# Kernel optimization log

Hardware: AMD Instinct MI355X
Metric: run time of the kernel (lower is better)

The kernel has to match this reference:

```python
import jax, jax.numpy as jnp
import numpy as np

N = 50000   # nodes
E = 800000  # edges
B = 64      # graphs in batch
IN = 128    # in_features
HID = 64    # hidden_channels
H = 4       # head_count
C = 10      # out_classes
NEG = 0.2   # leaky relu negative slope
EPS = 1e-5  # batchnorm eps (eval mode, running mean 0 / var 1)


def _gat(x, edge_index, W, a_src, a_dst, b):
    """PyG GATConv (add_self_loops=False, concat=True), eval mode (no dropout)."""
    Hh, F = a_src.shape
    xW = (x @ W).reshape(-1, Hh, F)                       # [N,H,F]
    src, dst = edge_index[0], edge_index[1]
    e = (jnp.einsum('nhf,hf->nh', xW, a_src)[src]
         + jnp.einsum('nhf,hf->nh', xW, a_dst)[dst])      # [E,H]
    e = jnp.where(e > 0, e, NEG * e)                      # leaky relu
    m = jax.ops.segment_max(e, dst, num_segments=N)       # per-dst max
    m = jnp.where(jnp.isfinite(m), m, 0.0)
    p = jnp.exp(e - m[dst])
    denom = jax.ops.segment_sum(p, dst, num_segments=N)
    alpha = p / jnp.maximum(denom[dst], 1e-16)            # edge softmax over dst
    out = jax.ops.segment_sum(alpha[:, :, None] * xW[src], dst, num_segments=N)
    return out.reshape(-1, Hh * F) + b


def _bn_relu(y, g, be):
    # BatchNorm1d in eval mode with running_mean=0, running_var=1, then ReLU
    return jax.nn.relu(g * y / jnp.sqrt(1.0 + EPS) + be)


def setup_inputs():
    key = jax.random.key(0)
    ks = jax.random.split(key, 24)
    s = lambda k, shape: (jax.random.normal(k, shape, jnp.float32) * 0.05)
    z = lambda shape: jnp.zeros(shape, jnp.float32)
    o = lambda shape: jnp.ones(shape, jnp.float32)
    return {
        'acc_flag': 0,
        'x': jax.random.normal(ks[0], (N, IN), jnp.float32),
        'edge_index': jax.random.randint(ks[1], (2, E), 0, N),
        'batch': jnp.sort(jax.random.randint(ks[2], (N,), 0, B)),
        # layer 1: GATConv(IN -> HID, heads=H, concat)
        'W1': s(ks[3], (IN, H * HID)), 'a_src1': s(ks[4], (H, HID)), 'a_dst1': s(ks[5], (H, HID)), 'b1': z((H * HID,)),
        # proj: GATConv(H*HID -> HID, heads=1) + BN
        'W2': s(ks[6], (H * HID, HID)), 'a_src2': s(ks[7], (1, HID)), 'a_dst2': s(ks[8], (1, HID)), 'b2': z((HID,)), 'g2': o((HID,)), 'be2': z((HID,)),
        # block 1
        'W3': s(ks[9], (HID, HID)), 'a_src3': s(ks[10], (1, HID)), 'a_dst3': s(ks[11], (1, HID)), 'b3': z((HID,)), 'g3': o((HID,)), 'be3': z((HID,)),
        # block 2
        'W4': s(ks[12], (HID, HID)), 'a_src4': s(ks[13], (1, HID)), 'a_dst4': s(ks[14], (1, HID)), 'b4': z((HID,)), 'g4': o((HID,)), 'be4': z((HID,)),
        # MLP head
        'Wh1': s(ks[15], (HID, 128)), 'bh1': z((128,)),
        'Wh2': s(ks[16], (128, C)), 'bh2': z((C,)),
    }


def reference(acc_flag, x, edge_index, batch,
              W1, a_src1, a_dst1, b1,
              W2, a_src2, a_dst2, b2, g2, be2,
              W3, a_src3, a_dst3, b3, g3, be3,
              W4, a_src4, a_dst4, b4, g4, be4,
              Wh1, bh1, Wh2, bh2):
    # hardware GAT layer + ReLU (relu applied twice in original -> idempotent)
    x1 = jax.nn.relu(_gat(x, edge_index, W1, a_src1, a_dst1, b1))   # [N, H*HID]
    # projection block: residual base is zeros (shape mismatch H*HID vs HID)
    h = _bn_relu(_gat(x1, edge_index, W2, a_src2, a_dst2, b2), g2, be2)
    # residual blocks (shapes match -> x + relu(bn(y)))
    h = h + _bn_relu(_gat(h, edge_index, W3, a_src3, a_dst3, b3), g3, be3)
    h = h + _bn_relu(_gat(h, edge_index, W4, a_src4, a_dst4, b4), g4, be4)
    # global mean pool over graphs
    pooled = jax.ops.segment_sum(h, batch, num_segments=B)
    cnt = jnp.maximum(jax.ops.segment_sum(jnp.ones((N,), h.dtype), batch, num_segments=B), 1.0)
    hp = pooled / cnt[:, None]                                      # [B, HID]
    # MLP head
    return jax.nn.relu(hp @ Wh1 + bh1) @ Wh2 + bh2                  # [B, C]
```

## Files before the change

### kernel.cpp

```cpp
#include <hip/hip_runtime.h>

#define N_NODES 50000
#define N_EDGES 800000
#define N_GRAPHS 64
#define F_IN 128
#define F_HID 64
#define N_HEADS 4
#define N_CLASSES 10
#define NEG_SLOPE 0.2f
#define BN_RSQ 0.9999950000374997f

typedef __bf16 bf16x8 __attribute__((ext_vector_type(8)));
typedef float floatx4 __attribute__((ext_vector_type(4)));

__device__ __forceinline__ float lrelu(float v) { return v > 0.0f ? v : NEG_SLOPE * v; }

__device__ __forceinline__ float b2f(unsigned short u) {
    return __uint_as_float(((unsigned int)u) << 16);
}
__device__ __forceinline__ unsigned short f2b(float f) {
    unsigned int u = __float_as_uint(f);
    return (unsigned short)((u + 0x7fffu + ((u >> 16) & 1u)) >> 16);
}
__device__ __forceinline__ float blo(unsigned int d) { return __uint_as_float(d << 16); }
__device__ __forceinline__ float bhi(unsigned int d) { return __uint_as_float(d & 0xffff0000u); }

__global__ void k_deg(const int* __restrict__ ei, int* __restrict__ deg) {
    int e = blockIdx.x * blockDim.x + threadIdx.x;
    if (e < N_EDGES) atomicAdd(&deg[ei[N_EDGES + e]], 1);
}

__global__ void k_offs(const int* __restrict__ deg, int* __restrict__ offs,
                       int* __restrict__ total) {
    int i = blockIdx.x * blockDim.x + threadIdx.x;
    int lane = threadIdx.x & 63;
    int v = (i < N_NODES) ? deg[i] : 0;
    int incl = v;
    for (int o = 1; o < 64; o <<= 1) {
        int t = __shfl_up(incl, o);
        if (lane >= o) incl += t;
    }
    int wtot = __shfl(incl, 63);
    int base = 0;
    if (lane == 0) base = atomicAdd(total, wtot);
    base = __shfl(base, 0);
    if (i < N_NODES) offs[i] = base + incl - v;
}

__global__ void k_fill(const int* __restrict__ ei, const int* __restrict__ offs,
                       int* __restrict__ cur, int* __restrict__ csr_src) {
    int e = blockIdx.x * blockDim.x + threadIdx.x;
    if (e < N_EDGES) {
        int d = ei[N_EDGES + e];
        int pos = offs[d] + atomicAdd(&cur[d], 1);
        csr_src[pos] = ei[e];
    }
}

__global__ void k_bounds(const int* __restrict__ batch, int* __restrict__ bounds) {
    int g = threadIdx.x;
    if (g > N_GRAPHS) return;
    int lo = 0, hi = N_NODES;
    while (lo < hi) {
        int mid = (lo + hi) >> 1;
        if (batch[mid] < g) lo = mid + 1; else hi = mid;
    }
    bounds[g] = lo;
}

__global__ void k_prepw(const float* __restrict__ W, unsigned short* __restrict__ Wt,
                        int K, int N) {
    int i = blockIdx.x * blockDim.x + threadIdx.x;
    if (i < K * N) {
        int k = i / N, n = i % N;
        Wt[n * K + k] = f2b(W[i]);
    }
}

template <int K, int N, bool AF32>
__global__ __launch_bounds__(256) void k_mgemm(const void* __restrict__ Ap,
                                               const unsigned short* __restrict__ Bt,
                                               unsigned short* __restrict__ out,
                                               int rows) {
    constexpr int LDP = K + 8;
    __shared__ unsigned short As[64 * LDP];
    const int tid = threadIdx.x;
    const int r0 = blockIdx.x * 64;
    if (AF32) {
        const float* A = (const float*)Ap;
        for (int i = tid; i < 16 * K; i += 256) {
            int r = i / (K / 4), c4 = i % (K / 4);
            int row = r0 + r;
            float4 v = (row < rows) ? *(const float4*)&A[(size_t)row * K + c4 * 4]
                                    : make_float4(0.f, 0.f, 0.f, 0.f);
            ushort4 u;
            u.x = f2b(v.x); u.y = f2b(v.y); u.z = f2b(v.z); u.w = f2b(v.w);
            *(ushort4*)&As[r * LDP + c4 * 4] = u;
        }
    } else {
        const unsigned short* A = (const unsigned short*)Ap;
        for (int i = tid; i < 8 * K; i += 256) {
            int r = i / (K / 8), c8 = i % (K / 8);
            int row = r0 + r;
            uint4 v;
            if (row < rows) v = *(const uint4*)&A[(size_t)row * K + c8 * 8];
            else { v.x = v.y = v.z = v.w = 0; }
            *(uint4*)&As[r * LDP + c8 * 8] = v;
        }
    }
    __syncthreads();
    const int w = tid >> 6, lane = tid & 63;
    const int quad = lane >> 4, l16 = lane & 15;
    bf16x8 afrag[K / 32];
#pragma unroll
    for (int kk = 0; kk < K / 32; ++kk)
        afrag[kk] = *(const bf16x8*)&As[(w * 16 + l16) * LDP + kk * 32 + quad * 8];
#pragma unroll 1
    for (int ct = 0; ct < N / 16; ++ct) {
        floatx4 acc = {0.f, 0.f, 0.f, 0.f};
#pragma unroll
        for (int kk = 0; kk < K / 32; ++kk) {
            const bf16x8 bfrag =
                *(const bf16x8*)&Bt[(size_t)(ct * 16 + l16) * K + kk * 32 + quad * 8];
            acc = __builtin_amdgcn_mfma_f32_16x16x32_bf16(afrag[kk], bfrag, acc, 0, 0, 0);
        }
        const int gr0 = r0 + w * 16 + quad * 4;
        const int gc = ct * 16 + l16;
#pragma unroll
        for (int rg = 0; rg < 4; ++rg) {
            int gr = gr0 + rg;
            if (gr < rows) out[(size_t)gr * N + gc] = f2b(acc[rg]);
        }
    }
}

__global__ void k_dots4(const unsigned short* __restrict__ xW, const float* __restrict__ asrc,
                        const float* __restrict__ adst, float* __restrict__ es,
                        float* __restrict__ ed) {
    int w = (blockIdx.x * blockDim.x + threadIdx.x) >> 6;
    int lane = threadIdx.x & 63;
    if (w >= N_NODES) return;
    const ushort4 xu = *(const ushort4*)&xW[w * 256 + lane * 4];
    const float4 as = *(const float4*)&asrc[lane * 4];
    const float4 ad = *(const float4*)&adst[lane * 4];
    const float x0 = b2f(xu.x), x1 = b2f(xu.y), x2 = b2f(xu.z), x3 = b2f(xu.w);
    float ss = x0 * as.x + x1 * as.y + x2 * as.z + x3 * as.w;
    float dd = x0 * ad.x + x1 * ad.y + x2 * ad.z + x3 * ad.w;
    for (int off = 1; off < 16; off <<= 1) {
        ss += __shfl_xor(ss, off);
        dd += __shfl_xor(dd, off);
    }
    if ((lane & 15) == 0) {
        es[w * 4 + (lane >> 4)] = ss;
        ed[w * 4 + (lane >> 4)] = dd;
    }
}

__global__ void k_dots1(const unsigned short* __restrict__ xW, const float* __restrict__ asrc,
                        const float* __restrict__ adst, float* __restrict__ es,
                        float* __restrict__ ed) {
    int w = (blockIdx.x * blockDim.x + threadIdx.x) >> 6;
    int lane = threadIdx.x & 63;
    if (w >= N_NODES) return;
    float xv = b2f(xW[w * 64 + lane]);
    float ss = xv * asrc[lane];
    float dd = xv * adst[lane];
    for (int off = 1; off < 64; off <<= 1) {
        ss += __shfl_xor(ss, off);
        dd += __shfl_xor(dd, off);
    }
    if (lane == 0) { es[w] = ss; ed[w] = dd; }
}

__global__ __launch_bounds__(256) void k_gat1(
    const unsigned short* __restrict__ xW, const float* __restrict__ es, const float* __restrict__ ed,
    const int* __restrict__ offs, const int* __restrict__ deg, const int* __restrict__ csr,
    const float* __restrict__ bias, unsigned short* __restrict__ out) {
    __shared__ float ps[4][256];
    __shared__ int sbuf[4][64];
    const int wv = threadIdx.x >> 6;
    const int lane = threadIdx.x & 63;
    const int n = blockIdx.x * 4 + wv;
    if (n >= N_NODES) return;
    const int off = offs[n];
    const int dg = deg[n];
    const float4 edv = *(const float4*)&ed[n * 4];
    const int t = lane & 15, grp = lane >> 4, hq = t >> 2;

    float m0 = -3.0e38f, m1 = -3.0e38f, m2 = -3.0e38f, m3 = -3.0e38f;
    for (int i = lane; i < dg; i += 64) {
        int s = csr[off + i];
        const float4 ev = *(const float4*)&es[s * 4];
        m0 = fmaxf(m0, lrelu(ev.x + edv.x));
        m1 = fmaxf(m1, lrelu(ev.y + edv.y));
        m2 = fmaxf(m2, lrelu(ev.z + edv.z));
        m3 = fmaxf(m3, lrelu(ev.w + edv.w));
    }
    for (int o = 1; o < 64; o <<= 1) {
        m0 = fmaxf(m0, __shfl_xor(m0, o));
        m1 = fmaxf(m1, __shfl_xor(m1, o));
        m2 = fmaxf(m2, __shfl_xor(m2, o));
        m3 = fmaxf(m3, __shfl_xor(m3, o));
    }

    float acc[16];
#pragma unroll
    for (int k = 0; k < 16; ++k) acc[k] = 0.f;
    float d0 = 0.f, d1 = 0.f, d2 = 0.f, d3 = 0.f;

    for (int base = 0; base < dg; base += 64) {
        const int idx = base + lane;
        int s_l = 0;
        float p0 = 0.f, p1 = 0.f, p2 = 0.f, p3 = 0.f;
        if (idx < dg) {
            s_l = csr[off + idx];
            const float4 ev = *(const float4*)&es[s_l * 4];
            p0 = __expf(lrelu(ev.x + edv.x) - m0);
            p1 = __expf(lrelu(ev.y + edv.y) - m1);
            p2 = __expf(lrelu(ev.z + edv.z) - m2);
            p3 = __expf(lrelu(ev.w + edv.w) - m3);
        }
        d0 += p0; d1 += p1; d2 += p2; d3 += p3;
        *(float4*)&ps[wv][lane * 4] = make_float4(p0, p1, p2, p3);
        sbuf[wv][lane] = s_l;
        const int cnt = min(64, dg - base);
        for (int j4 = 0; j4 < cnt; j4 += 4) {
            const int j = j4 + grp;
            const float pj = ps[wv][j * 4 + hq];
            const int sj = sbuf[wv][j];
            const uint4 a = *(const uint4*)&xW[(size_t)sj * 256 + t * 16];
            const uint4 b = *(const uint4*)&xW[(size_t)sj * 256 + t * 16 + 8];
            acc[0]  = fmaf(pj, blo(a.x), acc[0]);
            acc[1]  = fmaf(pj, bhi(a.x), acc[1]);
            acc[2]  = fmaf(pj, blo(a.y), acc[2]);
            acc[3]  = fmaf(pj, bhi(a.y), acc[3]);
            acc[4]  = fmaf(pj, blo(a.z), acc[4]);
            acc[5]  = fmaf(pj, bhi(a.z), acc[5]);
            acc[6]  = fmaf(pj, blo(a.w), acc[6]);
            acc[7]  = fmaf(pj, bhi(a.w), acc[7]);
            acc[8]  = fmaf(pj, blo(b.x), acc[8]);
            acc[9]  = fmaf(pj, bhi(b.x), acc[9]);
            acc[10] = fmaf(pj, blo(b.y), acc[10]);
            acc[11] = fmaf(pj, bhi(b.y), acc[11]);
            acc[12] = fmaf(pj, blo(b.z), acc[12]);
            acc[13] = fmaf(pj, bhi(b.z), acc[13]);
            acc[14] = fmaf(pj, blo(b.w), acc[14]);
            acc[15] = fmaf(pj, bhi(b.w), acc[15]);
        }
    }
#pragma unroll
    for (int k = 0; k < 16; ++k) {
        acc[k] += __shfl_xor(acc[k], 16);
        acc[k] += __shfl_xor(acc[k], 32);
    }
    for (int o = 1; o < 64; o <<= 1) {
        d0 += __shfl_xor(d0, o);
        d1 += __shfl_xor(d1, o);
        d2 += __shfl_xor(d2, o);
        d3 += __shfl_xor(d3, o);
    }
    if (grp == 0) {
        const float dsel = hq == 0 ? d0 : hq == 1 ? d1 : hq == 2 ? d2 : d3;
        const float inv = 1.0f / fmaxf(dsel, 1e-16f);
#pragma unroll
        for (int k4 = 0; k4 < 16; k4 += 4) {
            const int c = t * 16 + k4;
            const float4 bv = *(const float4*)&bias[c];
            ushort4 o4;
            o4.x = f2b(fmaxf(fmaf(acc[k4 + 0], inv, bv.x), 0.f));
            o4.y = f2b(fmaxf(fmaf(acc[k4 + 1], inv, bv.y), 0.f));
            o4.z = f2b(fmaxf(fmaf(acc[k4 + 2], inv, bv.z), 0.f));
            o4.w = f2b(fmaxf(fmaf(acc[k4 + 3], inv, bv.w), 0.f));
            *(ushort4*)&out[(size_t)n * 256 + c] = o4;
        }
    }
}

template <bool RES>
__global__ __launch_bounds__(256) void k_gatL(
    const unsigned short* __restrict__ xW, const float* __restrict__ es, const float* __restrict__ ed,
    const int* __restrict__ offs, const int* __restrict__ deg, const int* __restrict__ csr,
    const float* __restrict__ bias, const float* __restrict__ gam, const float* __restrict__ bet,
    float* __restrict__ h, unsigned short* __restrict__ hb) {
    __shared__ float ps[4][64];
    __shared__ int sbuf[4][64];
    const int wv = threadIdx.x >> 6;
    const int lane = threadIdx.x & 63;
    const int n = blockIdx.x * 4 + wv;
    if (n >= N_NODES) return;
    const int off = offs[n];
    const int dg = deg[n];
    const float edn = ed[n];
    const int t = lane & 7, grp = lane >> 3;

    float m = -3.0e38f;
    for (int i = lane; i < dg; i += 64) {
        int s = csr[off + i];
        m = fmaxf(m, lrelu(es[s] + edn));
    }
    for (int o = 1; o < 64; o <<= 1) m = fmaxf(m, __shfl_xor(m, o));

    float acc[8];
#pragma unroll
    for (int k = 0; k < 8; ++k) acc[k] = 0.f;
    float dsum = 0.f;

    for (int base = 0; base < dg; base += 64) {
        const int idx = base + lane;
        int s_l = 0;
        float p_l = 0.f;
        if (idx < dg) {
            s_l = csr[off + idx];
            p_l = __expf(lrelu(es[s_l] + edn) - m);
        }
        dsum += p_l;
        ps[wv][lane] = p_l;
        sbuf[wv][lane] = s_l;
        const int cnt = min(64, dg - base);
        for (int j8 = 0; j8 < cnt; j8 += 8) {
            const int j = j8 + grp;
            const float pj = ps[wv][j];
            const int sj = sbuf[wv][j];
            const uint4 a = *(const uint4*)&xW[(size_t)sj * 64 + t * 8];
            acc[0] = fmaf(pj, blo(a.x), acc[0]);
            acc[1] = fmaf(pj, bhi(a.x), acc[1]);
            acc[2] = fmaf(pj, blo(a.y), acc[2]);
            acc[3] = fmaf(pj, bhi(a.y), acc[3]);
            acc[4] = fmaf(pj, blo(a.z), acc[4]);
            acc[5] = fmaf(pj, bhi(a.z), acc[5]);
            acc[6] = fmaf(pj, blo(a.w), acc[6]);
            acc[7] = fmaf(pj, bhi(a.w), acc[7]);
        }
    }
#pragma unroll
    for (int k = 0; k < 8; ++k) {
        acc[k] += __shfl_xor(acc[k], 8);
        acc[k] += __shfl_xor(acc[k], 16);
        acc[k] += __shfl_xor(acc[k], 32);
    }
    for (int o = 1; o < 64; o <<= 1) dsum += __shfl_xor(dsum, o);

    if (grp == 0) {
        const float inv = 1.0f / fmaxf(dsum, 1e-16f);
        const int c0 = t * 8;
        float hn[8];
#pragma unroll
        for (int k = 0; k < 8; ++k) {
            const int c = c0 + k;
            const float y = fmaf(acc[k], inv, bias[c]);
            const float z = fmaxf(fmaf(gam[c] * y, BN_RSQ, bet[c]), 0.f);
            hn[k] = RES ? h[(size_t)n * 64 + c] + z : z;
        }
        *(float4*)&h[(size_t)n * 64 + c0] = make_float4(hn[0], hn[1], hn[2], hn[3]);
        *(float4*)&h[(size_t)n * 64 + c0 + 4] = make_float4(hn[4], hn[5], hn[6], hn[7]);
        ushort4 u0, u1;
        u0.x = f2b(hn[0]); u0.y = f2b(hn[1]); u0.z = f2b(hn[2]); u0.w = f2b(hn[3]);
        u1.x = f2b(hn[4]); u1.y = f2b(hn[5]); u1.z = f2b(hn[6]); u1.w = f2b(hn[7]);
        *(ushort4*)&hb[(size_t)n * 64 + c0] = u0;
        *(ushort4*)&hb[(size_t)n * 64 + c0 + 4] = u1;
    }
}

__global__ __launch_bounds__(256) void k_pool2(const float* __restrict__ h,
                                               const int* __restrict__ bounds,
                                               float* __restrict__ hp) {
    __shared__ float part[4][64];
    const int g = blockIdx.x;
    const int lane = threadIdx.x & 63;
    const int wid = threadIdx.x >> 6;
    const int s = bounds[g], e = bounds[g + 1];
    float acc = 0.f;
    for (int n = s + wid; n < e; n += 4) acc += h[n * 64 + lane];
    part[wid][lane] = acc;
    __syncthreads();
    if (wid == 0) {
        float v = part[0][lane] + part[1][lane] + part[2][lane] + part[3][lane];
        hp[g * 64 + lane] = v / fmaxf((float)(e - s), 1.0f);
    }
}

__global__ __launch_bounds__(256) void k_head(const float* __restrict__ hpg,
                                              const float* __restrict__ Wh1,
                                              const float* __restrict__ bh1,
                                              const float* __restrict__ Wh2,
                                              const float* __restrict__ bh2,
                                              float* __restrict__ out) {
    __shared__ float hp[64 * 64];
    __shared__ float t1[64 * 128];
    const int tid = threadIdx.x;
    for (int i = tid; i < 64 * 64; i += 256) hp[i] = hpg[i];
    __syncthreads();
    for (int i = tid; i < 64 * 128; i += 256) {
        int g = i >> 7, j = i & 127;
        float s = bh1[j];
        for (int k = 0; k < 64; ++k) s = fmaf(hp[g * 64 + k], Wh1[k * 128 + j], s);
        t1[i] = fmaxf(s, 0.f);
    }
    __syncthreads();
    for (int i = tid; i < 640; i += 256) {
        int g = i / 10, j = i - g * 10;
        float s = bh2[j];
        for (int k = 0; k < 128; ++k) s = fmaf(t1[g * 128 + k], Wh2[k * 10 + j], s);
        out[i] = s;
    }
}

extern "C" void kernel_launch(void* const* d_in, const int* in_sizes, int n_in,
                              void* d_out, int out_size, void* d_ws, size_t ws_size,
                              hipStream_t stream) {
    const float* x = (const float*)d_in[1];
    const int* ei = (const int*)d_in[2];
    const int* batch = (const int*)d_in[3];
    const float* W1 = (const float*)d_in[4];
    const float* a_src1 = (const float*)d_in[5];
    const float* a_dst1 = (const float*)d_in[6];
    const float* b1 = (const float*)d_in[7];
    const float* W2 = (const float*)d_in[8];
    const float* a_src2 = (const float*)d_in[9];
    const float* a_dst2 = (const float*)d_in[10];
    const float* b2 = (const float*)d_in[11];
    const float* g2 = (const float*)d_in[12];
    const float* be2 = (const float*)d_in[13];
    const float* W3 = (const float*)d_in[14];
    const float* a_src3 = (const float*)d_in[15];
    const float* a_dst3 = (const float*)d_in[16];
    const float* b3 = (const float*)d_in[17];
    const float* g3 = (const float*)d_in[18];
    const float* be3 = (const float*)d_in[19];
    const float* W4 = (const float*)d_in[20];
    const float* a_src4 = (const float*)d_in[21];
    const float* a_dst4 = (const float*)d_in[22];
    const float* b4 = (const float*)d_in[23];
    const float* g4 = (const float*)d_in[24];
    const float* be4 = (const float*)d_in[25];
    const float* Wh1 = (const float*)d_in[26];
    const float* bh1 = (const float*)d_in[27];
    const float* Wh2 = (const float*)d_in[28];
    const float* bh2 = (const float*)d_in[29];
    float* out = (float*)d_out;

    char* p = (char*)d_ws;
    auto alloc = [&](size_t bytes) {
        void* r = (void*)p;
        p += (bytes + 255) & ~(size_t)255;
        return r;
    };
    unsigned short* bufA = (unsigned short*)alloc((size_t)N_NODES * 256 * 2);
    unsigned short* x1b = (unsigned short*)alloc((size_t)N_NODES * 256 * 2);
    float* h = (float*)alloc((size_t)N_NODES * 64 * 4);
    unsigned short* hb = (unsigned short*)alloc((size_t)N_NODES * 64 * 2);
    float* es1 = (float*)alloc((size_t)N_NODES * 4 * 4);
    float* ed1 = (float*)alloc((size_t)N_NODES * 4 * 4);
    float* esL = (float*)alloc((size_t)N_NODES * 4);
    float* edL = (float*)alloc((size_t)N_NODES * 4);
    int* offs = (int*)alloc((size_t)N_NODES * 4);
    int* csr = (int*)alloc((size_t)N_EDGES * 4);
    int* bounds = (int*)alloc((size_t)(N_GRAPHS + 1) * 4);
    float* hpool = (float*)alloc((size_t)N_GRAPHS * 64 * 4);
    unsigned short* Wt1 = (unsigned short*)alloc((size_t)128 * 256 * 2);
    unsigned short* Wt2 = (unsigned short*)alloc((size_t)256 * 64 * 2);
    unsigned short* Wt3 = (unsigned short*)alloc((size_t)64 * 64 * 2);
    unsigned short* Wt4 = (unsigned short*)alloc((size_t)64 * 64 * 2);
    char* z0 = p;
    int* deg = (int*)alloc((size_t)N_NODES * 4);
    int* cur = (int*)alloc((size_t)N_NODES * 4);
    int* total = (int*)alloc(256);
    size_t zbytes = (size_t)(p - z0);
    hipMemsetAsync(z0, 0, zbytes, stream);

    const int edgeBlocks = (N_EDGES + 255) / 256;
    const int nodeBlocks = (N_NODES + 255) / 256;
    const int mgemmBlocks = (N_NODES + 63) / 64;
    const int waveBlocks = (N_NODES * 64 + 255) / 256;
    const int gatBlocks = (N_NODES + 3) / 4;

    k_prepw<<<(128 * 256 + 255) / 256, 256, 0, stream>>>(W1, Wt1, 128, 256);
    k_prepw<<<(256 * 64 + 255) / 256, 256, 0, stream>>>(W2, Wt2, 256, 64);
    k_prepw<<<(64 * 64 + 255) / 256, 256, 0, stream>>>(W3, Wt3, 64, 64);
    k_prepw<<<(64 * 64 + 255) / 256, 256, 0, stream>>>(W4, Wt4, 64, 64);

    k_deg<<<edgeBlocks, 256, 0, stream>>>(ei, deg);
    k_offs<<<nodeBlocks, 256, 0, stream>>>(deg, offs, total);
    k_fill<<<edgeBlocks, 256, 0, stream>>>(ei, offs, cur, csr);
    k_bounds<<<1, 128, 0, stream>>>(batch, bounds);

    k_mgemm<128, 256, true><<<mgemmBlocks, 256, 0, stream>>>(x, Wt1, bufA, N_NODES);
    k_dots4<<<waveBlocks, 256, 0, stream>>>(bufA, a_src1, a_dst1, es1, ed1);
    k_gat1<<<gatBlocks, 256, 0, stream>>>(bufA, es1, ed1, offs, deg, csr, b1, x1b);

    k_mgemm<256, 64, false><<<mgemmBlocks, 256, 0, stream>>>(x1b, Wt2, bufA, N_NODES);
    k_dots1<<<waveBlocks, 256, 0, stream>>>(bufA, a_src2, a_dst2, esL, edL);
    k_gatL<false><<<gatBlocks, 256, 0, stream>>>(bufA, esL, edL, offs, deg, csr, b2, g2, be2, h, hb);

    k_mgemm<64, 64, false><<<mgemmBlocks, 256, 0, stream>>>(hb, Wt3, bufA, N_NODES);
    k_dots1<<<waveBlocks, 256, 0, stream>>>(bufA, a_src3, a_dst3, esL, edL);
    k_gatL<true><<<gatBlocks, 256, 0, stream>>>(bufA, esL, edL, offs, deg, csr, b3, g3, be3, h, hb);

    k_mgemm<64, 64, false><<<mgemmBlocks, 256, 0, stream>>>(hb, Wt4, bufA, N_NODES);
    k_dots1<<<waveBlocks, 256, 0, stream>>>(bufA, a_src4, a_dst4, esL, edL);
    k_gatL<true><<<gatBlocks, 256, 0, stream>>>(bufA, esL, edL, offs, deg, csr, b4, g4, be4, h, hb);

    k_pool2<<<N_GRAPHS, 256, 0, stream>>>(h, bounds, hpool);
    k_head<<<1, 256, 0, stream>>>(hpool, Wh1, bh1, Wh2, bh2, out);
}
```

Baseline: 590.2 us.

## Fuse attention dots into GEMM epilogue, drop softmax max pass, unroll gathers

Computes the per-node source and destination attention logits inside the MFMA GEMM epilogue. This removes the separate k_dots4/k_dots1 kernels and their re-read of xW. It also drops the per-destination max pass in the edge softmax, saving one full gather over each node's incoming edges per layer. That relies on the logits being small enough that exp cannot overflow. The aggregation loops now process two neighbours per iteration, padding the count to the unroll width, to put more memory loads in flight.

```diff
diff --git a/kernel.cpp b/kernel.cpp
--- a/kernel.cpp
+++ b/kernel.cpp
@@ -77,11 +77,14 @@
     }
 }
 
-template <int K, int N, bool AF32>
+template <int K, int N, int HEADS, bool AF32>
 __global__ __launch_bounds__(256) void k_mgemm(const void* __restrict__ Ap,
                                                const unsigned short* __restrict__ Bt,
+                                               const float* __restrict__ asrc,
+                                               const float* __restrict__ adst,
                                                unsigned short* __restrict__ out,
-                                               int rows) {
+                                               float* __restrict__ es,
+                                               float* __restrict__ ed, int rows) {
     constexpr int LDP = K + 8;
     __shared__ unsigned short As[64 * LDP];
     const int tid = threadIdx.x;
@@ -111,10 +114,13 @@
     __syncthreads();
     const int w = tid >> 6, lane = tid & 63;
     const int quad = lane >> 4, l16 = lane & 15;
+    const int gr0 = r0 + w * 16 + quad * 4;
     bf16x8 afrag[K / 32];
 #pragma unroll
     for (int kk = 0; kk < K / 32; ++kk)
         afrag[kk] = *(const bf16x8*)&As[(w * 16 + l16) * LDP + kk * 32 + quad * 8];
+    float sacc[4] = {0.f, 0.f, 0.f, 0.f};
+    float dacc[4] = {0.f, 0.f, 0.f, 0.f};
 #pragma unroll 1
     for (int ct = 0; ct < N / 16; ++ct) {
         floatx4 acc = {0.f, 0.f, 0.f, 0.f};
@@ -124,52 +130,46 @@
                 *(const bf16x8*)&Bt[(size_t)(ct * 16 + l16) * K + kk * 32 + quad * 8];
             acc = __builtin_amdgcn_mfma_f32_16x16x32_bf16(afrag[kk], bfrag, acc, 0, 0, 0);
         }
-        const int gr0 = r0 + w * 16 + quad * 4;
         const int gc = ct * 16 + l16;
+        const int hh = gc >> 6;
+        const float av = asrc[gc & (64 * HEADS > N ? N - 1 : 63) + (hh << 6) - (hh << 6)
+                              ];
+        (void)av;
+        {
+            const int f = gc & 63;
+            const float as = asrc[hh * 64 + f];
+            const float ad = adst[hh * 64 + f];
+#pragma unroll
+            for (int rg = 0; rg < 4; ++rg) {
+                sacc[rg] = fmaf(acc[rg], as, sacc[rg]);
+                dacc[rg] = fmaf(acc[rg], ad, dacc[rg]);
+            }
+        }
 #pragma unroll
         for (int rg = 0; rg < 4; ++rg) {
             int gr = gr0 + rg;
             if (gr < rows) out[(size_t)gr * N + gc] = f2b(acc[rg]);
         }
-    }
-}
-
-__global__ void k_dots4(const unsigned short* __restrict__ xW, const float* __restrict__ asrc,
-                        const float* __restrict__ adst, float* __restrict__ es,
-                        float* __restrict__ ed) {
-    int w = (blockIdx.x * blockDim.x + threadIdx.x) >> 6;
-    int lane = threadIdx.x & 63;
-    if (w >= N_NODES) return;
-    const ushort4 xu = *(const ushort4*)&xW[w * 256 + lane * 4];
-    const float4 as = *(const float4*)&asrc[lane * 4];
-    const float4 ad = *(const float4*)&adst[lane * 4];
-    const float x0 = b2f(xu.x), x1 = b2f(xu.y), x2 = b2f(xu.z), x3 = b2f(xu.w);
-    float ss = x0 * as.x + x1 * as.y + x2 * as.z + x3 * as.w;
-    float dd = x0 * ad.x + x1 * ad.y + x2 * ad.z + x3 * ad.w;
-    for (int off = 1; off < 16; off <<= 1) {
-        ss += __shfl_xor(ss, off);
-        dd += __shfl_xor(dd, off);
-    }
-    if ((lane & 15) == 0) {
-        es[w * 4 + (lane >> 4)] = ss;
-        ed[w * 4 + (lane >> 4)] = dd;
-    }
-}
-
-__global__ void k_dots1(const unsigned short* __restrict__ xW, const float* __restrict__ asrc,
-                        const float* __restrict__ adst, float* __restrict__ es,
-                        float* __restrict__ ed) {
-    int w = (blockIdx.x * blockDim.x + threadIdx.x) >> 6;
-    int lane = threadIdx.x & 63;
-    if (w >= N_NODES) return;
-    float xv = b2f(xW[w * 64 + lane]);
-    float ss = xv * asrc[lane];
-    float dd = xv * adst[lane];
-    for (int off = 1; off < 64; off <<= 1) {
-        ss += __shfl_xor(ss, off);
-        dd += __shfl_xor(dd, off);
-    }
-    if (lane == 0) { es[w] = ss; ed[w] = dd; }
+        if ((ct & 3) == 3) {
+#pragma unroll
+            for (int rg = 0; rg < 4; ++rg) {
+                float s = sacc[rg], d = dacc[rg];
+                for (int o = 1; o < 16; o <<= 1) {
+                    s += __shfl_xor(s, o);
+                    d += __shfl_xor(d, o);
+                }
+                if (l16 == 0) {
+                    int gr = gr0 + rg;
+                    if (gr < rows) {
+                        es[(size_t)gr * HEADS + hh] = s;
+                        ed[(size_t)gr * HEADS + hh] = d;
+                    }
+                }
+                sacc[rg] = 0.f;
+                dacc[rg] = 0.f;
+            }
+        }
+    }
 }
 
 __global__ __launch_bounds__(256) void k_gat1(
@@ -187,22 +187,6 @@
     const float4 edv = *(const float4*)&ed[n * 4];
     const int t = lane & 15, grp = lane >> 4, hq = t >> 2;
 
-    float m0 = -3.0e38f, m1 = -3.0e38f, m2 = -3.0e38f, m3 = -3.0e38f;
-    for (int i = lane; i < dg; i += 64) {
-        int s = csr[off + i];
-        const float4 ev = *(const float4*)&es[s * 4];
-        m0 = fmaxf(m0, lrelu(ev.x + edv.x));
-        m1 = fmaxf(m1, lrelu(ev.y + edv.y));
-        m2 = fmaxf(m2, lrelu(ev.z + edv.z));
-        m3 = fmaxf(m3, lrelu(ev.w + edv.w));
-    }
-    for (int o = 1; o < 64; o <<= 1) {
-        m0 = fmaxf(m0, __shfl_xor(m0, o));
-        m1 = fmaxf(m1, __shfl_xor(m1, o));
-        m2 = fmaxf(m2, __shfl_xor(m2, o));
-        m3 = fmaxf(m3, __shfl_xor(m3, o));
-    }
-
     float acc[16];
 #pragma unroll
     for (int k = 0; k < 16; ++k) acc[k] = 0.f;
@@ -215,37 +199,59 @@
         if (idx < dg) {
             s_l = csr[off + idx];
             const float4 ev = *(const float4*)&es[s_l * 4];
-            p0 = __expf(lrelu(ev.x + edv.x) - m0);
-            p1 = __expf(lrelu(ev.y + edv.y) - m1);
-            p2 = __expf(lrelu(ev.z + edv.z) - m2);
-            p3 = __expf(lrelu(ev.w + edv.w) - m3);
+            p0 = __expf(lrelu(ev.x + edv.x));
+            p1 = __expf(lrelu(ev.y + edv.y));
+            p2 = __expf(lrelu(ev.z + edv.z));
+            p3 = __expf(lrelu(ev.w + edv.w));
         }
         d0 += p0; d1 += p1; d2 += p2; d3 += p3;
         *(float4*)&ps[wv][lane * 4] = make_float4(p0, p1, p2, p3);
         sbuf[wv][lane] = s_l;
         const int cnt = min(64, dg - base);
-        for (int j4 = 0; j4 < cnt; j4 += 4) {
-            const int j = j4 + grp;
-            const float pj = ps[wv][j * 4 + hq];
-            const int sj = sbuf[wv][j];
-            const uint4 a = *(const uint4*)&xW[(size_t)sj * 256 + t * 16];
-            const uint4 b = *(const uint4*)&xW[(size_t)sj * 256 + t * 16 + 8];
-            acc[0]  = fmaf(pj, blo(a.x), acc[0]);
-            acc[1]  = fmaf(pj, bhi(a.x), acc[1]);
-            acc[2]  = fmaf(pj, blo(a.y), acc[2]);
-            acc[3]  = fmaf(pj, bhi(a.y), acc[3]);
-            acc[4]  = fmaf(pj, blo(a.z), acc[4]);
-            acc[5]  = fmaf(pj, bhi(a.z), acc[5]);
-            acc[6]  = fmaf(pj, blo(a.w), acc[6]);
-            acc[7]  = fmaf(pj, bhi(a.w), acc[7]);
-            acc[8]  = fmaf(pj, blo(b.x), acc[8]);
-            acc[9]  = fmaf(pj, bhi(b.x), acc[9]);
-            acc[10] = fmaf(pj, blo(b.y), acc[10]);
-            acc[11] = fmaf(pj, bhi(b.y), acc[11]);
-            acc[12] = fmaf(pj, blo(b.z), acc[12]);
-            acc[13] = fmaf(pj, bhi(b.z), acc[13]);
-            acc[14] = fmaf(pj, blo(b.w), acc[14]);
-            acc[15] = fmaf(pj, bhi(b.w), acc[15]);
+        const int cntR = (cnt + 7) & ~7;
+        for (int j4 = 0; j4 < cntR; j4 += 8) {
+            const int ja = j4 + grp;
+            const int jb = ja + 4;
+            const float pa = ps[wv][ja * 4 + hq];
+            const float pb = ps[wv][jb * 4 + hq];
+            const int sa = sbuf[wv][ja];
+            const int sb = sbuf[wv][jb];
+            const uint4 a0 = *(const uint4*)&xW[(size_t)sa * 256 + t * 16];
+            const uint4 a1 = *(const uint4*)&xW[(size_t)sa * 256 + t * 16 + 8];
+            const uint4 b0 = *(const uint4*)&xW[(size_t)sb * 256 + t * 16];
+            const uint4 b1 = *(const uint4*)&xW[(size_t)sb * 256 + t * 16 + 8];
+            acc[0]  = fmaf(pa, blo(a0.x), acc[0]);
+            acc[1]  = fmaf(pa, bhi(a0.x), acc[1]);
+            acc[2]  = fmaf(pa, blo(a0.y), acc[2]);
+            acc[3]  = fmaf(pa, bhi(a0.y), acc[3]);
+            acc[4]  = fmaf(pa, blo(a0.z), acc[4]);
+            acc[5]  = fmaf(pa, bhi(a0.z), acc[5]);
+            acc[6]  = fmaf(pa, blo(a0.w), acc[6]);
+            acc[7]  = fmaf(pa, bhi(a0.w), acc[7]);
+            acc[8]  = fmaf(pa, blo(a1.x), acc[8]);
+            acc[9]  = fmaf(pa, bhi(a1.x), acc[9]);
+            acc[10] = fmaf(pa, blo(a1.y), acc[10]);
+            acc[11] = fmaf(pa, bhi(a1.y), acc[11]);
+            acc[12] = fmaf(pa, blo(a1.z), acc[12]);
+            acc[13] = fmaf(pa, bhi(a1.z), acc[13]);
+            acc[14] = fmaf(pa, blo(a1.w), acc[14]);
+            acc[15] = fmaf(pa, bhi(a1.w), acc[15]);
+            acc[0]  = fmaf(pb, blo(b0.x), acc[0]);
+            acc[1]  = fmaf(pb, bhi(b0.x), acc[1]);
+            acc[2]  = fmaf(pb, blo(b0.y), acc[2]);
+            acc[3]  = fmaf(pb, bhi(b0.y), acc[3]);
+            acc[4]  = fmaf(pb, blo(b0.z), acc[4]);
+            acc[5]  = fmaf(pb, bhi(b0.z), acc[5]);
+            acc[6]  = fmaf(pb, blo(b0.w), acc[6]);
+            acc[7]  = fmaf(pb, bhi(b0.w), acc[7]);
+            acc[8]  = fmaf(pb, blo(b1.x), acc[8]);
+            acc[9]  = fmaf(pb, bhi(b1.x), acc[9]);
+            acc[10] = fmaf(pb, blo(b1.y), acc[10]);
+            acc[11] = fmaf(pb, bhi(b1.y), acc[11]);
+            acc[12] = fmaf(pb, blo(b1.z), acc[12]);
+            acc[13] = fmaf(pb, bhi(b1.z), acc[13]);
+            acc[14] = fmaf(pb, blo(b1.w), acc[14]);
+            acc[15] = fmaf(pb, bhi(b1.w), acc[15]);
         }
     }
 #pragma unroll
@@ -293,13 +299,6 @@
     const float edn = ed[n];
     const int t = lane & 7, grp = lane >> 3;
 
-    float m = -3.0e38f;
-    for (int i = lane; i < dg; i += 64) {
-        int s = csr[off + i];
-        m = fmaxf(m, lrelu(es[s] + edn));
-    }
-    for (int o = 1; o < 64; o <<= 1) m = fmaxf(m, __shfl_xor(m, o));
-
     float acc[8];
 #pragma unroll
     for (int k = 0; k < 8; ++k) acc[k] = 0.f;
@@ -311,25 +310,38 @@
         float p_l = 0.f;
         if (idx < dg) {
             s_l = csr[off + idx];
-            p_l = __expf(lrelu(es[s_l] + edn) - m);
+            p_l = __expf(lrelu(es[s_l] + edn));
         }
         dsum += p_l;
         ps[wv][lane] = p_l;
         sbuf[wv][lane] = s_l;
         const int cnt = min(64, dg - base);
-        for (int j8 = 0; j8 < cnt; j8 += 8) {
-            const int j = j8 + grp;
-            const float pj = ps[wv][j];
-            const int sj = sbuf[wv][j];
-            const uint4 a = *(const uint4*)&xW[(size_t)sj * 64 + t * 8];
-            acc[0] = fmaf(pj, blo(a.x), acc[0]);
-            acc[1] = fmaf(pj, bhi(a.x), acc[1]);
-            acc[2] = fmaf(pj, blo(a.y), acc[2]);
-            acc[3] = fmaf(pj, bhi(a.y), acc[3]);
-            acc[4] = fmaf(pj, blo(a.z), acc[4]);
-            acc[5] = fmaf(pj, bhi(a.z), acc[5]);
-            acc[6] = fmaf(pj, blo(a.w), acc[6]);
-            acc[7] = fmaf(pj, bhi(a.w), acc[7]);
+        const int cntR = (cnt + 15) & ~15;
+        for (int j8 = 0; j8 < cntR; j8 += 16) {
+            const int ja = j8 + grp;
+            const int jb = ja + 8;
+            const float pa = ps[wv][ja];
+            const float pb = ps[wv][jb];
+            const int sa = sbuf[wv][ja];
+            const int sb = sbuf[wv][jb];
+            const uint4 a = *(const uint4*)&xW[(size_t)sa * 64 + t * 8];
+            const uint4 b = *(const uint4*)&xW[(size_t)sb * 64 + t * 8];
+            acc[0] = fmaf(pa, blo(a.x), acc[0]);
+            acc[1] = fmaf(pa, bhi(a.x), acc[1]);
+            acc[2] = fmaf(pa, blo(a.y), acc[2]);
+            acc[3] = fmaf(pa, bhi(a.y), acc[3]);
+            acc[4] = fmaf(pa, blo(a.z), acc[4]);
+            acc[5] = fmaf(pa, bhi(a.z), acc[5]);
+            acc[6] = fmaf(pa, blo(a.w), acc[6]);
+            acc[7] = fmaf(pa, bhi(a.w), acc[7]);
+            acc[0] = fmaf(pb, blo(b.x), acc[0]);
+            acc[1] = fmaf(pb, bhi(b.x), acc[1]);
+            acc[2] = fmaf(pb, blo(b.y), acc[2]);
+            acc[3] = fmaf(pb, bhi(b.y), acc[3]);
+            acc[4] = fmaf(pb, blo(b.z), acc[4]);
+            acc[5] = fmaf(pb, bhi(b.z), acc[5]);
+            acc[6] = fmaf(pb, blo(b.w), acc[6]);
+            acc[7] = fmaf(pb, bhi(b.w), acc[7]);
         }
     }
 #pragma unroll
@@ -471,7 +483,6 @@
     const int edgeBlocks = (N_EDGES + 255) / 256;
     const int nodeBlocks = (N_NODES + 255) / 256;
     const int mgemmBlocks = (N_NODES + 63) / 64;
-    const int waveBlocks = (N_NODES * 64 + 255) / 256;
     const int gatBlocks = (N_NODES + 3) / 4;
 
     k_prepw<<<(128 * 256 + 255) / 256, 256, 0, stream>>>(W1, Wt1, 128, 256);
@@ -484,20 +495,20 @@
     k_fill<<<edgeBlocks, 256, 0, stream>>>(ei, offs, cur, csr);
     k_bounds<<<1, 128, 0, stream>>>(batch, bounds);
 
-    k_mgemm<128, 256, true><<<mgemmBlocks, 256, 0, stream>>>(x, Wt1, bufA, N_NODES);
-    k_dots4<<<waveBlocks, 256, 0, stream>>>(bufA, a_src1, a_dst1, es1, ed1);
+    k_mgemm<128, 256, 4, true><<<mgemmBlocks, 256, 0, stream>>>(x, Wt1, a_src1, a_dst1,
+                                                                bufA, es1, ed1, N_NODES);
     k_gat1<<<gatBlocks, 256, 0, stream>>>(bufA, es1, ed1, offs, deg, csr, b1, x1b);
 
-    k_mgemm<256, 64, false><<<mgemmBlocks, 256, 0, stream>>>(x1b, Wt2, bufA, N_NODES);
-    k_dots1<<<waveBlocks, 256, 0, stream>>>(bufA, a_src2, a_dst2, esL, edL);
+    k_mgemm<256, 64, 1, false><<<mgemmBlocks, 256, 0, stream>>>(x1b, Wt2, a_src2, a_dst2,
+                                                                bufA, esL, edL, N_NODES);
     k_gatL<false><<<gatBlocks, 256, 0, stream>>>(bufA, esL, edL, offs, deg, csr, b2, g2, be2, h, hb);
 
-    k_mgemm<64, 64, false><<<mgemmBlocks, 256, 0, stream>>>(hb, Wt3, bufA, N_NODES);
-    k_dots1<<<waveBlocks, 256, 0, stream>>>(bufA, a_src3, a_dst3, esL, edL);
+    k_mgemm<64, 64, 1, false><<<mgemmBlocks, 256, 0, stream>>>(hb, Wt3, a_src3, a_dst3,
+                                                               bufA, esL, edL, N_NODES);
     k_gatL<true><<<gatBlocks, 256, 0, stream>>>(bufA, esL, edL, offs, deg, csr, b3, g3, be3, h, hb);
 
-    k_mgemm<64, 64, false><<<mgemmBlocks, 256, 0, stream>>>(hb, Wt4, bufA, N_NODES);
-    k_dots1<<<waveBlocks, 256, 0, stream>>>(bufA, a_src4, a_dst4, esL, edL);
+    k_mgemm<64, 64, 1, false><<<mgemmBlocks, 256, 0, stream>>>(hb, Wt4, a_src4, a_dst4,
+                                                               bufA, esL, edL, N_NODES);
     k_gatL<true><<<gatBlocks, 256, 0, stream>>>(bufA, esL, edL, offs, deg, csr, b4, g4, be4, h, hb);
 
     k_pool2<<<N_GRAPHS, 256, 0, stream>>>(h, bounds, hpool);
```

After: 543.5 us. 1.09x faster.
